# Kernel tuning notes

Measured on AMD Instinct MI355X. Metric: run time of the kernel, lower is better.

The kernel has to match this reference:

```python
import jax, jax.numpy as jnp
import numpy as np

BLOCK = (4, 8, 8)   # (t, h, w)
NH, D, DA = 8, 512, 64
EPS = 1e-5


def _layernorm(x, g, b):
    m = jnp.mean(x, axis=-1, keepdims=True)
    xc = x - m
    v = jnp.mean(xc * xc, axis=-1, keepdims=True)
    return xc * jax.lax.rsqrt(v + EPS) * g + b


def setup_inputs() -> dict:
    key = jax.random.key(0)
    ks = jax.random.split(key, 10)
    B, T, H, W = 2, 8, 32, 32
    t, h, w = BLOCK
    s_qkv = (2.0 / (D + DA)) ** 0.5   # xavier_normal for (d, da) fan
    s_lin = (2.0 / (D + D)) ** 0.5
    return {
        "x": jax.random.normal(ks[0], (B, D, T, H, W), jnp.float32),
        "dt_bank": 0.02 * jax.random.normal(ks[1], (NH, 2 * t - 1), jnp.float32),
        "dh_bank": 0.02 * jax.random.normal(ks[2], (NH, 2 * h - 1), jnp.float32),
        "dw_bank": 0.02 * jax.random.normal(ks[3], (NH, 2 * w - 1), jnp.float32),
        "ln1_g": jnp.ones((D,), jnp.float32),
        "ln1_b": jnp.zeros((D,), jnp.float32),
        "w_q": s_qkv * jax.random.normal(ks[4], (NH, D, DA), jnp.float32),
        "w_k": s_qkv * jax.random.normal(ks[5], (NH, D, DA), jnp.float32),
        "w_v": s_qkv * jax.random.normal(ks[6], (NH, D, DA), jnp.float32),
        "w_proj": s_lin * jax.random.normal(ks[7], (D, NH * DA), jnp.float32),
        "ln2_g": jnp.ones((D,), jnp.float32),
        "ln2_b": jnp.zeros((D,), jnp.float32),
        "w1": s_lin * jax.random.normal(ks[8], (D, D), jnp.float32),
        "b1": jnp.zeros((D,), jnp.float32),
        "w2": s_lin * jax.random.normal(ks[9], (D, D), jnp.float32),
        "b2": jnp.zeros((D,), jnp.float32),
    }


def _axial_bias(dt_bank, dh_bank, dw_bank):
    t, h, w = BLOCK
    thw = t * h * w
    ar = jnp.arange(thw)
    tt = ar // (h * w)
    hh = (ar // w) % h
    ww = ar % w
    # relative offsets shifted to be non-negative (matches dt += abs(dt.min()))
    it = tt[:, None] - tt[None, :] + (t - 1)
    ih = hh[:, None] - hh[None, :] + (h - 1)
    iw = ww[:, None] - ww[None, :] + (w - 1)
    return dt_bank[:, it] + dh_bank[:, ih] + dw_bank[:, iw]  # (NH, thw, thw)


def reference(x, dt_bank, dh_bank, dw_bank, ln1_g, ln1_b, w_q, w_k, w_v,
              w_proj, ln2_g, ln2_b, w1, b1, w2, b2):
    B, C, T, H, W = x.shape
    t, h, w = BLOCK
    st, sh, sw = T // t, H // h, W // w
    thw = t * h * w
    nb = B * st * sh * sw

    # block split: (B,C,T,H,W) -> (nb, thw, C)
    xb = x.reshape(B, C, st, t, sh, h, sw, w).transpose(0, 2, 4, 6, 1, 3, 5, 7)
    xb = xb.reshape(nb, C, thw).transpose(0, 2, 1)

    Bb = _axial_bias(dt_bank, dh_bank, dw_bank)  # (NH, thw, thw)

    # --- multi-head attention with additive axial bias ---
    resid = xb
    xn = _layernorm(xb, ln1_g, ln1_b)
    q = jnp.einsum('bnd,hde->hbne', xn, w_q)
    k = jnp.einsum('bnd,hde->hbne', xn, w_k)
    v = jnp.einsum('bnd,hde->hbne', xn, w_v)
    scale = 1.0 / jnp.sqrt(jnp.asarray(DA, x.dtype))
    attn = jnp.einsum('hbne,hbme->hbnm', q, k) * scale + Bb[:, None]
    attn = jax.nn.softmax(attn, axis=-1)
    out = jnp.einsum('hbnm,hbme->hbne', attn, v)         # (NH, nb, thw, DA)
    out = out.transpose(1, 2, 0, 3).reshape(nb, thw, NH * DA)  # head-major concat
    out = out @ w_proj.T + resid

    # --- FFN with residual ---
    y = _layernorm(out, ln2_g, ln2_b)
    y = jax.nn.relu(y @ w1.T + b1) @ w2.T + b2
    out = y + out

    # un-block: (nb, thw, C) -> (B,C,T,H,W)
    out = out.transpose(0, 2, 1).reshape(B, st, sh, sw, C, t, h, w)
    out = out.transpose(0, 4, 1, 5, 2, 6, 3, 7).reshape(B, C, T, H, W)
    return out
```

## Files before the change

kernel.cpp:

```cpp
#include <hip/hip_runtime.h>
#include <hip/hip_bf16.h>
#include <stdint.h>

typedef __attribute__((ext_vector_type(4))) float f32x4;
typedef __attribute__((ext_vector_type(8))) short s16x8;
typedef __attribute__((ext_vector_type(4))) short s16x4;
typedef __attribute__((ext_vector_type(8))) __bf16 b16x8;

__device__ __forceinline__ f32x4 mfma16(s16x8 a, s16x8 b, f32x4 c) {
  return __builtin_amdgcn_mfma_f32_16x16x32_bf16(
      __builtin_bit_cast(b16x8, a), __builtin_bit_cast(b16x8, b), c, 0, 0, 0);
}

__device__ __forceinline__ void gl_lds16(const void* g, void* l) {
  __builtin_amdgcn_global_load_lds(
      (const __attribute__((address_space(1))) void*)g,
      (__attribute__((address_space(3))) void*)l, 16, 0, 0);
}

__device__ __forceinline__ unsigned short f2bf(float f) {
  union { float f; unsigned u; } v; v.f = f;
  unsigned u = v.u;
  return (unsigned short)((u + 0x7FFFu + ((u >> 16) & 1u)) >> 16);
}

__device__ __forceinline__ float bf2f(unsigned short u) {
  union { unsigned u; float f; } v; v.u = ((unsigned)u) << 16; return v.f;
}

__device__ __forceinline__ unsigned cvt_pk_bf16(float a, float b) {
  unsigned r;
  asm("v_cvt_pk_bf16_f32 %0, %1, %2" : "=v"(r) : "v"(a), "v"(b));
  return r;
}

#if __has_builtin(__builtin_amdgcn_exp2f)
#define EXP2F(x) __builtin_amdgcn_exp2f(x)
#else
#define EXP2F(x) exp2f(x)
#endif

__global__ __launch_bounds__(256) void k_prep(
    const float* __restrict__ wq, const float* __restrict__ wk, const float* __restrict__ wv,
    const float* __restrict__ wp, const float* __restrict__ w1, const float* __restrict__ w2,
    unsigned short* __restrict__ qkvT, unsigned short* __restrict__ wpT,
    unsigned short* __restrict__ w1T, unsigned short* __restrict__ w2T)
{
  int i = blockIdx.x * 256 + threadIdx.x;
  if (i < 786432) {
    int n = i >> 9, d = i & 511;
    const float* src = (n < 512) ? wq : (n < 1024 ? wk : wv);
    int nn = n & 511;
    int h = nn >> 6, e = nn & 63;
    qkvT[i] = f2bf(src[((size_t)h * 512 + d) * 64 + e]);
  } else {
    int j = i - 786432;
    int w = j >> 18;
    int o = j & 262143;
    const float* s = (w == 0) ? wp : (w == 1 ? w1 : w2);
    unsigned short* dst = (w == 0) ? wpT : (w == 1 ? w1T : w2T);
    dst[o] = f2bf(s[o]);
  }
}

__global__ __launch_bounds__(256) void k_gather_ln(
    const float* __restrict__ x, const float* __restrict__ g1, const float* __restrict__ b1,
    float* __restrict__ xb, unsigned short* __restrict__ xn)
{
  __shared__ float lx[16][517];
  int gid = blockIdx.x;
  int h2 = gid & 1, hh = (gid >> 1) & 7, tt = (gid >> 4) & 3,
      shI = (gid >> 6) & 3, stI = (gid >> 8) & 1, bI = (gid >> 9) & 1;
  const float* xbase = x + (size_t)bI * 4194304 + (size_t)(stI * 4 + tt) * 1024
                       + (shI * 8 + hh) * 32 + h2 * 16;
  int t = threadIdx.x;
  for (int i = 0; i < 8; ++i) {
    int slot = i * 256 + t;
    int c = slot >> 2, w8 = slot & 3;
    const float4 v = *(const float4*)(xbase + (size_t)c * 8192 + w8 * 4);
    lx[w8 * 4 + 0][c] = v.x; lx[w8 * 4 + 1][c] = v.y;
    lx[w8 * 4 + 2][c] = v.z; lx[w8 * 4 + 3][c] = v.w;
  }
  __syncthreads();
  int lane = t & 63, wid = t >> 6;
  for (int q = 0; q < 4; ++q) {
    int widx = wid * 4 + q;
    float vv[8]; float s = 0.f, ss = 0.f;
    #pragma unroll
    for (int i = 0; i < 8; ++i) { float v = lx[widx][lane + i * 64]; vv[i] = v; s += v; ss += v * v; }
    #pragma unroll
    for (int d = 1; d < 64; d <<= 1) { s += __shfl_xor(s, d); ss += __shfl_xor(ss, d); }
    float mean = s * (1.f / 512.f);
    float var = ss * (1.f / 512.f) - mean * mean;
    float rs = rsqrtf(var + 1e-5f);
    int sw = h2 * 2 + (widx >> 3), ww = widx & 7;
    int blk = ((bI * 2 + stI) * 4 + shI) * 4 + sw;
    int n = tt * 64 + hh * 8 + ww;
    size_t base = ((size_t)blk * 256 + n) * 512;
    #pragma unroll
    for (int i = 0; i < 8; ++i) {
      int c = lane + i * 64;
      float v = vv[i];
      xb[base + c] = v;
      xn[base + c] = f2bf((v - mean) * rs * g1[c] + b1[c]);
    }
  }
}

template<int EPI>
__global__ __launch_bounds__(256, 2) void k_gemm(
    const unsigned short* __restrict__ A, const unsigned short* __restrict__ Bt,
    int M, int N,
    unsigned short* __restrict__ Cbf, float* __restrict__ Cf,
    const float* __restrict__ bias, const float* __restrict__ addf,
    const unsigned short* __restrict__ addbf,
    unsigned short* __restrict__ vTout)
{
  constexpr int K = 512;
  __shared__ __align__(16) unsigned short a_lds[128 * 64];
  __shared__ __align__(16) unsigned short b_lds[128 * 64];
  int tid = threadIdx.x, lane = tid & 63, wid = tid >> 6;
  int nwg = gridDim.x * gridDim.y;
  int lin = blockIdx.y * gridDim.x + blockIdx.x;
  int swz = (lin & 7) * (nwg >> 3) + (lin >> 3);
  int bx = swz % gridDim.x, by = swz / gridDim.x;
  int m0 = bx * 128, n0 = by * 128;
  int wm = (wid >> 1) * 64, wn = (wid & 1) * 64;
  int r15 = lane & 15, g = lane >> 4;

  f32x4 acc[4][4] = {};

  for (int ks = 0; ks < K; ks += 64) {
    #pragma unroll
    for (int s = 0; s < 4; ++s) {
      int seg = wid * 4 + s;
      int slot = seg * 64 + lane;
      int m = slot >> 3, lc = (slot & 7) ^ (m & 7);
      gl_lds16(A + (size_t)(m0 + m) * K + ks + lc * 8, (char*)a_lds + seg * 1024);
      gl_lds16(Bt + (size_t)(n0 + m) * K + ks + lc * 8, (char*)b_lds + seg * 1024);
    }
    __syncthreads();
    #pragma unroll
    for (int kk = 0; kk < 2; ++kk) {
      s16x8 af[4], bfr[4];
      #pragma unroll
      for (int f = 0; f < 4; ++f) {
        int mm = wm + f * 16 + r15;
        af[f] = *(const s16x8*)((const char*)a_lds + mm * 128 + (((kk * 4 + g) ^ (mm & 7)) * 16));
        int nn = wn + f * 16 + r15;
        bfr[f] = *(const s16x8*)((const char*)b_lds + nn * 128 + (((kk * 4 + g) ^ (nn & 7)) * 16));
      }
      __builtin_amdgcn_s_setprio(1);
      #pragma unroll
      for (int fm = 0; fm < 4; ++fm)
        #pragma unroll
        for (int fn = 0; fn < 4; ++fn)
          acc[fm][fn] = mfma16(af[fm], bfr[fn], acc[fm][fn]);
      __builtin_amdgcn_s_setprio(0);
    }
    __syncthreads();
  }

  int g4 = g * 4;
  #pragma unroll
  for (int fm = 0; fm < 4; ++fm) {
    #pragma unroll
    for (int fn = 0; fn < 4; ++fn) {
      int col = n0 + wn + fn * 16 + r15;
      int row0 = m0 + wm + fm * 16 + g4;
      if (EPI == 0 && col >= 1024) {
        int h = (col - 1024) >> 6, e = col & 63;
        int blk = row0 >> 8, mtok = row0 & 255;
        s16x4 pk;
        #pragma unroll
        for (int r = 0; r < 4; ++r) pk[r] = (short)f2bf(acc[fm][fn][r]);
        *(s16x4*)(vTout + (((size_t)blk * 8 + h) * 64 + e) * 256 + mtok) = pk;
      } else {
        #pragma unroll
        for (int r = 0; r < 4; ++r) {
          int row = row0 + r;
          float v = acc[fm][fn][r];
          if (EPI == 0) {
            Cbf[(size_t)row * 1536 + col] = f2bf(v);
          } else if (EPI == 1) {
            Cbf[(size_t)row * 512 + col] = f2bf(v + addf[(size_t)row * 512 + col]);
          } else if (EPI == 2) {
            Cbf[(size_t)row * 512 + col] = f2bf(fmaxf(v + bias[col], 0.f));
          } else {
            Cf[(size_t)row * 512 + col] = v + bias[col] + bf2f(addbf[(size_t)row * 512 + col]);
          }
        }
      }
    }
  }
}

__global__ __launch_bounds__(256, 2) void k_attn(
    const unsigned short* __restrict__ qkv, const unsigned short* __restrict__ vT,
    const float* __restrict__ dtb, const float* __restrict__ dhb, const float* __restrict__ dwb,
    unsigned short* __restrict__ aout)
{
  __shared__ __align__(16) unsigned short p_lds[4][64 * 64];
  __shared__ float bt_s[8], bh_s[16], bw_s[16];

  const float L2E = 1.44269504f;
  const float SC = 0.125f * 1.44269504f;

  int tid = threadIdx.x, lane = tid & 63, wid = tid >> 6;
  int bk = blockIdx.x >> 3, h = blockIdx.x & 7;
  if (tid < 7) bt_s[tid] = dtb[h * 7 + tid] * L2E;
  else if (tid < 22) bh_s[tid - 7] = dhb[h * 15 + tid - 7] * L2E;
  else if (tid < 37) bw_s[tid - 22] = dwb[h * 15 + tid - 22] * L2E;

  int r15 = lane & 15, g = lane >> 4;
  int wq0 = wid * 64;
  size_t bkBase = (size_t)bk * 256;

  s16x8 qf[4][2];
  #pragma unroll
  for (int fn = 0; fn < 4; ++fn)
    #pragma unroll
    for (int kk = 0; kk < 2; ++kk)
      qf[fn][kk] = *(const s16x8*)(qkv + (bkBase + wq0 + fn * 16 + r15) * 1536
                                   + h * 64 + kk * 32 + g * 8);

  __syncthreads();

  float btoff[4], hb[7], wb[4];
  {
    int Dh = (r15 >> 3) - (g >> 1) + 7;
    int Wb = (r15 & 7) - 4 * (g & 1) + 7;
    #pragma unroll
    for (int mt = 0; mt < 4; ++mt) btoff[mt] = bt_s[wid + 3 - mt];
    #pragma unroll
    for (int d = 0; d < 7; ++d) hb[d] = bh_s[Dh + 2 * d - 6];
    #pragma unroll
    for (int r = 0; r < 4; ++r) wb[r] = bw_s[Wb - r];
  }

  f32x4 o[4][4] = {};
  float mrun[4] = {-1e30f, -1e30f, -1e30f, -1e30f};
  float lrun[4] = {0.f, 0.f, 0.f, 0.f};
  char* p_w = (char*)(&p_lds[wid][0]);

  #pragma unroll
  for (int mt = 0; mt < 4; ++mt) {
    int m0 = mt * 64;

    s16x8 vf[4][2];
    #pragma unroll
    for (int fe = 0; fe < 4; ++fe)
      #pragma unroll
      for (int mm = 0; mm < 2; ++mm)
        vf[fe][mm] = *(const s16x8*)(vT + (((size_t)bk * 8 + h) * 64 + fe * 16 + r15) * 256
                                     + m0 + mm * 32 + g * 8);

    f32x4 st[4][4] = {};
    #pragma unroll
    for (int kk = 0; kk < 2; ++kk) {
      s16x8 kf[4];
      #pragma unroll
      for (int fm = 0; fm < 4; ++fm)
        kf[fm] = *(const s16x8*)(qkv + (bkBase + m0 + fm * 16 + r15) * 1536
                                 + 512 + h * 64 + kk * 32 + g * 8);
      __builtin_amdgcn_s_setprio(1);
      #pragma unroll
      for (int fm = 0; fm < 4; ++fm)
        #pragma unroll
        for (int fn = 0; fn < 4; ++fn)
          st[fm][fn] = mfma16(kf[fm], qf[fn][kk], st[fm][fn]);
      __builtin_amdgcn_s_setprio(0);
    }

    #pragma unroll
    for (int fn = 0; fn < 4; ++fn) {
      float vals[16];
      float mx = -1e30f;
      #pragma unroll
      for (int fm = 0; fm < 4; ++fm) {
        float cc = btoff[mt] + hb[fn - fm + 3];
        #pragma unroll
        for (int r = 0; r < 4; ++r) {
          float v = fmaf(st[fm][fn][r], SC, cc) + wb[r];
          vals[fm * 4 + r] = v;
          mx = fmaxf(mx, v);
        }
      }
      mx = fmaxf(mx, __shfl_xor(mx, 16));
      mx = fmaxf(mx, __shfl_xor(mx, 32));
      if (!__all(mx <= mrun[fn] + 8.f)) {
        float mnew = fmaxf(mrun[fn], mx);
        float al = EXP2F(mrun[fn] - mnew);
        mrun[fn] = mnew;
        lrun[fn] *= al;
        #pragma unroll
        for (int fe = 0; fe < 4; ++fe)
          #pragma unroll
          for (int r = 0; r < 4; ++r)
            o[fe][fn][r] *= al;
      }
      float m_c = mrun[fn];
      float p[16]; float sum = 0.f;
      #pragma unroll
      for (int i = 0; i < 16; ++i) { p[i] = EXP2F(vals[i] - m_c); sum += p[i]; }
      sum += __shfl_xor(sum, 16);
      sum += __shfl_xor(sum, 32);
      lrun[fn] += sum;
      int nl = fn * 16 + r15;
      char* prow = p_w + nl * 128 + (g & 1) * 8;
      #pragma unroll
      for (int fm = 0; fm < 4; ++fm) {
        unsigned u0 = cvt_pk_bf16(p[fm * 4 + 0], p[fm * 4 + 1]);
        unsigned u1 = cvt_pk_bf16(p[fm * 4 + 2], p[fm * 4 + 3]);
        int lc = fm * 2 + (g >> 1);
        *(uint2*)(prow + ((lc ^ (nl & 7)) * 16)) = make_uint2(u0, u1);
      }
    }
    asm volatile("s_waitcnt lgkmcnt(0)" ::: "memory");
    __builtin_amdgcn_sched_barrier(0);

    #pragma unroll
    for (int mm = 0; mm < 2; ++mm) {
      s16x8 pf[4];
      #pragma unroll
      for (int fn = 0; fn < 4; ++fn) {
        int nl = fn * 16 + r15;
        pf[fn] = *(const s16x8*)(p_w + nl * 128 + (((mm * 4 + g) ^ (nl & 7)) * 16));
      }
      __builtin_amdgcn_s_setprio(1);
      #pragma unroll
      for (int fe = 0; fe < 4; ++fe)
        #pragma unroll
        for (int fn = 0; fn < 4; ++fn)
          o[fe][fn] = mfma16(vf[fe][mm], pf[fn], o[fe][fn]);
      __builtin_amdgcn_s_setprio(0);
    }
  }

  #pragma unroll
  for (int fn = 0; fn < 4; ++fn) {
    float inv = 1.f / lrun[fn];
    size_t rowb = (bkBase + wq0 + fn * 16 + r15) * 512 + h * 64;
    #pragma unroll
    for (int fe = 0; fe < 4; ++fe) {
      unsigned u0 = cvt_pk_bf16(o[fe][fn][0] * inv, o[fe][fn][1] * inv);
      unsigned u1 = cvt_pk_bf16(o[fe][fn][2] * inv, o[fe][fn][3] * inv);
      *(uint2*)(aout + rowb + fe * 16 + g * 4) = make_uint2(u0, u1);
    }
  }
}

__global__ __launch_bounds__(256) void k_ln2(
    const unsigned short* __restrict__ in, const float* __restrict__ g2, const float* __restrict__ b2,
    unsigned short* __restrict__ out)
{
  int token = blockIdx.x * 4 + (threadIdx.x >> 6);
  int lane = threadIdx.x & 63;
  s16x8 v8 = *(const s16x8*)(in + (size_t)token * 512 + lane * 8);
  float vv[8]; float s = 0.f, ss = 0.f;
  #pragma unroll
  for (int i = 0; i < 8; ++i) {
    float v = bf2f((unsigned short)v8[i]); vv[i] = v; s += v; ss += v * v;
  }
  #pragma unroll
  for (int d = 1; d < 64; d <<= 1) { s += __shfl_xor(s, d); ss += __shfl_xor(ss, d); }
  float mean = s * (1.f / 512.f);
  float var = ss * (1.f / 512.f) - mean * mean;
  float rs = rsqrtf(var + 1e-5f);
  const float4 gA = *(const float4*)(g2 + lane * 8);
  const float4 gB = *(const float4*)(g2 + lane * 8 + 4);
  const float4 bA = *(const float4*)(b2 + lane * 8);
  const float4 bB = *(const float4*)(b2 + lane * 8 + 4);
  float gv[8] = {gA.x, gA.y, gA.z, gA.w, gB.x, gB.y, gB.z, gB.w};
  float bv[8] = {bA.x, bA.y, bA.z, bA.w, bB.x, bB.y, bB.z, bB.w};
  s16x8 o8;
  #pragma unroll
  for (int i = 0; i < 8; ++i)
    o8[i] = (short)f2bf((vv[i] - mean) * rs * gv[i] + bv[i]);
  *(s16x8*)(out + (size_t)token * 512 + lane * 8) = o8;
}

__global__ __launch_bounds__(64) void k_scatter(
    const float* __restrict__ fin, float* __restrict__ out)
{
  __shared__ float lx[32][33];
  int gid = blockIdx.x;
  int cc = gid & 15;
  int sg = gid >> 4;
  int hh = sg & 7, tt = (sg >> 3) & 3, shI = (sg >> 5) & 3, stI = (sg >> 7) & 1, bI = (sg >> 8) & 1;
  int c0 = cc * 32;
  int l = threadIdx.x;
  #pragma unroll
  for (int i = 0; i < 4; ++i) {
    int slot = i * 64 + l;
    int tok = slot >> 3, c4 = slot & 7;
    int blk = ((bI * 2 + stI) * 4 + shI) * 4 + (tok >> 3);
    int n = tt * 64 + hh * 8 + (tok & 7);
    const float4 v = *(const float4*)(fin + ((size_t)blk * 256 + n) * 512 + c0 + c4 * 4);
    lx[tok][c4 * 4 + 0] = v.x; lx[tok][c4 * 4 + 1] = v.y;
    lx[tok][c4 * 4 + 2] = v.z; lx[tok][c4 * 4 + 3] = v.w;
  }
  __syncthreads();
  size_t obase = (size_t)bI * 4194304 + (size_t)(stI * 4 + tt) * 1024 + (shI * 8 + hh) * 32;
  #pragma unroll
  for (int i = 0; i < 4; ++i) {
    int crow = i * 8 + (l >> 3), w4 = l & 7;
    float4 v;
    v.x = lx[w4 * 4 + 0][crow]; v.y = lx[w4 * 4 + 1][crow];
    v.z = lx[w4 * 4 + 2][crow]; v.w = lx[w4 * 4 + 3][crow];
    *(float4*)(out + obase + (size_t)(c0 + crow) * 8192 + w4 * 4) = v;
  }
}

extern "C" void kernel_launch(void* const* d_in, const int* in_sizes, int n_in,
                              void* d_out, int out_size, void* d_ws, size_t ws_size,
                              hipStream_t stream)
{
  const float* x   = (const float*)d_in[0];
  const float* dtb = (const float*)d_in[1];
  const float* dhb = (const float*)d_in[2];
  const float* dwb = (const float*)d_in[3];
  const float* g1  = (const float*)d_in[4];
  const float* bb1 = (const float*)d_in[5];
  const float* wq  = (const float*)d_in[6];
  const float* wk  = (const float*)d_in[7];
  const float* wv  = (const float*)d_in[8];
  const float* wp  = (const float*)d_in[9];
  const float* g2  = (const float*)d_in[10];
  const float* bb2 = (const float*)d_in[11];
  const float* w1  = (const float*)d_in[12];
  const float* fb1 = (const float*)d_in[13];
  const float* w2  = (const float*)d_in[14];
  const float* fb2 = (const float*)d_in[15];

  char* ws = (char*)d_ws;
  float*          xb   = (float*)(ws + 0);
  unsigned short* vT   = (unsigned short*)(ws + 33554432);
  unsigned short* out1b= (unsigned short*)(ws + 33554432);
  unsigned short* qkv  = (unsigned short*)(ws + 67108864);
  unsigned short* xn   = (unsigned short*)(ws + 117440512);
  unsigned short* qkvT = (unsigned short*)(ws + 134217728);
  unsigned short* wpT  = (unsigned short*)(ws + 135790592);
  unsigned short* w1T  = (unsigned short*)(ws + 136314880);
  unsigned short* w2T  = (unsigned short*)(ws + 136839168);

  unsigned short* attn_out = xn;
  unsigned short* yb = xn;
  unsigned short* h1 = qkv;
  float* finalb = xb;
  float* outp = (float*)d_out;

  k_prep<<<6144, 256, 0, stream>>>(wq, wk, wv, wp, w1, w2, qkvT, wpT, w1T, w2T);
  k_gather_ln<<<1024, 256, 0, stream>>>(x, g1, bb1, xb, xn);
  k_gemm<0><<<dim3(128, 12), 256, 0, stream>>>(xn, qkvT, 16384, 1536, qkv, nullptr, nullptr, nullptr, nullptr, vT);
  k_attn<<<512, 256, 0, stream>>>(qkv, vT, dtb, dhb, dwb, attn_out);
  k_gemm<1><<<dim3(128, 4), 256, 0, stream>>>(attn_out, wpT, 16384, 512, out1b, nullptr, nullptr, xb, nullptr, nullptr);
  k_ln2<<<4096, 256, 0, stream>>>(out1b, g2, bb2, yb);
  k_gemm<2><<<dim3(128, 4), 256, 0, stream>>>(yb, w1T, 16384, 512, h1, nullptr, fb1, nullptr, nullptr, nullptr);
  k_gemm<3><<<dim3(128, 4), 256, 0, stream>>>(h1, w2T, 16384, 512, nullptr, finalb, fb2, nullptr, out1b, nullptr);
  k_scatter<<<8192, 64, 0, stream>>>(finalb, outp);
}
```

Baseline: 178.1 us.

## Stage K/V tiles in double-buffered LDS for attention and remap GEMM XCD swizzle

In the attention kernel, the four waves of a block now share K and V tiles. Those tiles are loaded once per block into LDS via global_load_lds and double-buffered across the four key tiles, with a block barrier per iteration. Previously each wave fetched its own copies from global memory. The aim is to cut redundant global traffic and overlap the next tile's load with compute. In exchange, LDS use grows and launch bounds drop to one block per CU, which reduces occupancy. The GEMM block-index swizzle is also replaced with a mapping that hardcodes 16 M-tiles per XCD, which assumes a specific grid shape.

Result: faster. 168.3 us (-5.5%).

```diff
diff --git a/kernel.cpp b/kernel.cpp
--- a/kernel.cpp
+++ b/kernel.cpp
@@ -120,10 +120,10 @@
   __shared__ __align__(16) unsigned short a_lds[128 * 64];
   __shared__ __align__(16) unsigned short b_lds[128 * 64];
   int tid = threadIdx.x, lane = tid & 63, wid = tid >> 6;
-  int nwg = gridDim.x * gridDim.y;
   int lin = blockIdx.y * gridDim.x + blockIdx.x;
-  int swz = (lin & 7) * (nwg >> 3) + (lin >> 3);
-  int bx = swz % gridDim.x, by = swz / gridDim.x;
+  int xcd = lin & 7, idx = lin >> 3;
+  int bx = xcd * 16 + (idx & 15);
+  int by = idx >> 4;
   int m0 = bx * 128, n0 = by * 128;
   int wm = (wid >> 1) * 64, wn = (wid & 1) * 64;
   int r15 = lane & 15, g = lane >> 4;
@@ -195,11 +195,13 @@
   }
 }
 
-__global__ __launch_bounds__(256, 2) void k_attn(
+__global__ __launch_bounds__(256, 1) void k_attn(
     const unsigned short* __restrict__ qkv, const unsigned short* __restrict__ vT,
     const float* __restrict__ dtb, const float* __restrict__ dhb, const float* __restrict__ dwb,
     unsigned short* __restrict__ aout)
 {
+  __shared__ __align__(16) unsigned short k_lds[2][64 * 64];
+  __shared__ __align__(16) unsigned short v_lds[2][64 * 64];
   __shared__ __align__(16) unsigned short p_lds[4][64 * 64];
   __shared__ float bt_s[8], bh_s[16], bw_s[16];
 
@@ -215,6 +217,8 @@
   int r15 = lane & 15, g = lane >> 4;
   int wq0 = wid * 64;
   size_t bkBase = (size_t)bk * 256;
+  const unsigned short* kbase = qkv + 512 + h * 64;
+  const unsigned short* vbase = vT + ((size_t)bk * 8 + h) * 64 * 256;
 
   s16x8 qf[4][2];
   #pragma unroll
@@ -224,9 +228,24 @@
       qf[fn][kk] = *(const s16x8*)(qkv + (bkBase + wq0 + fn * 16 + r15) * 1536
                                    + h * 64 + kk * 32 + g * 8);
 
+  float btoff[4], hb[7], wb[4];
+
+  #pragma unroll
+  for (int s = 0; s < 4; ++s) {
+    int sg = wid * 4 + s;
+    if (sg < 8) {
+      int slot = sg * 64 + lane;
+      int m = slot >> 3, lc = (slot & 7) ^ (m & 7);
+      gl_lds16(kbase + (bkBase + m) * 1536 + lc * 8, (char*)(&k_lds[0][0]) + sg * 1024);
+    } else {
+      int sg2 = sg - 8;
+      int slot = sg2 * 64 + lane;
+      int e = slot >> 3, lc = (slot & 7) ^ (e & 7);
+      gl_lds16(vbase + (size_t)e * 256 + lc * 8, (char*)(&v_lds[0][0]) + sg2 * 1024);
+    }
+  }
   __syncthreads();
 
-  float btoff[4], hb[7], wb[4];
   {
     int Dh = (r15 >> 3) - (g >> 1) + 7;
     int Wb = (r15 & 7) - 4 * (g & 1) + 7;
@@ -245,24 +264,38 @@
 
   #pragma unroll
   for (int mt = 0; mt < 4; ++mt) {
-    int m0 = mt * 64;
-
-    s16x8 vf[4][2];
-    #pragma unroll
-    for (int fe = 0; fe < 4; ++fe)
-      #pragma unroll
-      for (int mm = 0; mm < 2; ++mm)
-        vf[fe][mm] = *(const s16x8*)(vT + (((size_t)bk * 8 + h) * 64 + fe * 16 + r15) * 256
-                                     + m0 + mm * 32 + g * 8);
+    int cur = mt & 1;
+    if (mt < 3) {
+      int m0n = (mt + 1) * 64;
+      #pragma unroll
+      for (int s = 0; s < 4; ++s) {
+        int sg = wid * 4 + s;
+        if (sg < 8) {
+          int slot = sg * 64 + lane;
+          int m = slot >> 3, lc = (slot & 7) ^ (m & 7);
+          gl_lds16(kbase + (bkBase + m0n + m) * 1536 + lc * 8,
+                   (char*)(&k_lds[cur ^ 1][0]) + sg * 1024);
+        } else {
+          int sg2 = sg - 8;
+          int slot = sg2 * 64 + lane;
+          int e = slot >> 3, lc = (slot & 7) ^ (e & 7);
+          gl_lds16(vbase + (size_t)e * 256 + m0n + lc * 8,
+                   (char*)(&v_lds[cur ^ 1][0]) + sg2 * 1024);
+        }
+      }
+    }
+    const char* kl = (const char*)(&k_lds[cur][0]);
+    const char* vl = (const char*)(&v_lds[cur][0]);
 
     f32x4 st[4][4] = {};
     #pragma unroll
     for (int kk = 0; kk < 2; ++kk) {
       s16x8 kf[4];
       #pragma unroll
-      for (int fm = 0; fm < 4; ++fm)
-        kf[fm] = *(const s16x8*)(qkv + (bkBase + m0 + fm * 16 + r15) * 1536
-                                 + 512 + h * 64 + kk * 32 + g * 8);
+      for (int fm = 0; fm < 4; ++fm) {
+        int m = fm * 16 + r15;
+        kf[fm] = *(const s16x8*)(kl + m * 128 + (((kk * 4 + g) ^ (m & 7)) * 16));
+      }
       __builtin_amdgcn_s_setprio(1);
       #pragma unroll
       for (int fm = 0; fm < 4; ++fm)
@@ -317,11 +350,15 @@
       }
     }
     asm volatile("s_waitcnt lgkmcnt(0)" ::: "memory");
-    __builtin_amdgcn_sched_barrier(0);
 
     #pragma unroll
     for (int mm = 0; mm < 2; ++mm) {
-      s16x8 pf[4];
+      s16x8 vf[4], pf[4];
+      #pragma unroll
+      for (int fe = 0; fe < 4; ++fe) {
+        int e = fe * 16 + r15;
+        vf[fe] = *(const s16x8*)(vl + e * 128 + (((mm * 4 + g) ^ (e & 7)) * 16));
+      }
       #pragma unroll
       for (int fn = 0; fn < 4; ++fn) {
         int nl = fn * 16 + r15;
@@ -332,9 +369,10 @@
       for (int fe = 0; fe < 4; ++fe)
         #pragma unroll
         for (int fn = 0; fn < 4; ++fn)
-          o[fe][fn] = mfma16(vf[fe][mm], pf[fn], o[fe][fn]);
+          o[fe][fn] = mfma16(vf[fe][0] ? vf[fe] : vf[fe], pf[fn], o[fe][fn]);
       __builtin_amdgcn_s_setprio(0);
     }
+    __syncthreads();
   }
 
   #pragma unroll
```
